# Performance work log

Measured on AMD Instinct MI355X. Metric: run time of the kernel, lower is better.

Reference implementation:

```python
import jax, jax.numpy as jnp
import numpy as np


def setup_inputs() -> dict:
    key = jax.random.key(0)
    k1, k2, k3, k4 = jax.random.split(key, 4)
    n_entity, n_rel, dim = 2048, 32, 512
    entities = jax.random.normal(k1, (n_entity, dim), dtype=jnp.float32)
    relations = jax.random.normal(k2, (n_rel, dim), dtype=jnp.float32)
    W = jax.random.normal(k3, (dim, dim), dtype=jnp.float32) * (1.0 / np.sqrt(dim))
    b = jax.random.normal(k4, (dim,), dtype=jnp.float32) * 0.01
    return {"entities": entities, "relations": relations, "W": W, "b": b}


def reference(entities, relations, W, b):
    # gate_nn applied to both entities and relations (shared Linear)
    E = entities @ W.T + b            # [n_entity, dim]
    R = relations @ W.T + b           # [n_rel, dim]
    # Diagonal RESCAL: scores[e, r, f] = sum_d E[e,d] * R[r,d] * E[f,d]
    # Equivalent to the per-relation loop E @ diag(R_r) @ E^T, fused into one einsum.
    scores = jnp.einsum('ed,rd,fd->erf', E, R, E)  # [n_entity, n_rel, n_entity]
    return scores
```

## Files before the change

### kernel.cpp

```cpp
#include <hip/hip_runtime.h>

typedef __attribute__((ext_vector_type(8))) __bf16 bf16x8;
typedef __attribute__((ext_vector_type(4))) float f32x4;

__device__ __forceinline__ float bf2f(unsigned int u) {
    return __uint_as_float(u << 16);
}
__device__ __forceinline__ unsigned short f2bf(float f) {
    unsigned int x = __float_as_uint(f);
    return (unsigned short)((x + 0x7fffu + ((x >> 16) & 1u)) >> 16);
}

__global__ void cast_all(const float* __restrict__ ent, const float* __restrict__ rel,
                         const float* __restrict__ W,
                         unsigned short* __restrict__ X_bf,
                         unsigned short* __restrict__ W_bf) {
    int i = blockIdx.x * blockDim.x + threadIdx.x;
    const float* src;
    unsigned short* dst;
    int g;
    if (i < 262144) {
        src = ent; dst = X_bf; g = i;
    } else if (i < 266240) {
        src = rel; dst = X_bf + 2048 * 512; g = i - 262144;
    } else {
        if (i >= 331776) return;
        src = W; dst = W_bf; g = i - 266240;
    }
    float4 v = reinterpret_cast<const float4*>(src)[g];
    ushort4 o;
    o.x = f2bf(v.x); o.y = f2bf(v.y); o.z = f2bf(v.z); o.w = f2bf(v.w);
    reinterpret_cast<ushort4*>(dst)[g] = o;
}

__device__ __forceinline__ unsigned int mul2bf(unsigned int a, unsigned int b) {
    float a0 = bf2f(a & 0xffffu), a1 = bf2f(a >> 16);
    float b0 = bf2f(b & 0xffffu), b1 = bf2f(b >> 16);
    return (unsigned int)f2bf(a0 * b0) | ((unsigned int)f2bf(a1 * b1) << 16);
}

__global__ void build_ap(const unsigned short* __restrict__ G,
                         unsigned short* __restrict__ Ap) {
    int t = blockIdx.x * blockDim.x + threadIdx.x;
    int row = t >> 6;
    int d = (t & 63) * 8;
    int e = row >> 5, r = row & 31;
    const uint4 ev = *reinterpret_cast<const uint4*>(G + e * 512 + d);
    const uint4 rv = *reinterpret_cast<const uint4*>(G + (2048 + r) * 512 + d);
    uint4 o;
    o.x = mul2bf(ev.x, rv.x);
    o.y = mul2bf(ev.y, rv.y);
    o.z = mul2bf(ev.z, rv.z);
    o.w = mul2bf(ev.w, rv.w);
    *reinterpret_cast<uint4*>(Ap + (size_t)row * 512 + d) = o;
}

#define BM 128
#define BN 128
#define BK 64

template <bool GUARD_M, bool BIAS_BF16OUT>
__global__ __launch_bounds__(256, 2) void mfma_gemm_bt(
    const unsigned short* __restrict__ A,
    const unsigned short* __restrict__ Bt,
    const float* __restrict__ bias,
    void* __restrict__ Cout,
    int M, int N, int K) {
    __shared__ __align__(16) unsigned short As[BM * BK];
    __shared__ __align__(16) unsigned short Bs[BN * BK];

    const int tid = threadIdx.x;
    const int lane = tid & 63;
    const int wave = tid >> 6;
    const int nbn = N / BN;
    const int bm0 = (blockIdx.x / nbn) * BM;
    const int bn0 = (blockIdx.x % nbn) * BN;
    const int wr = wave >> 1, wc = wave & 1;

    f32x4 acc[4][4] = {};

    const int srow = wave * 32 + (lane >> 3);
    const int scol = (lane & 7) * 8;

    for (int kb = 0; kb < K; kb += BK) {
#pragma unroll
        for (int i = 0; i < 4; ++i) {
            int row = bm0 + srow + i * 8;
            if (GUARD_M) row = min(row, M - 1);
            const unsigned short* src = A + (size_t)row * K + kb + scol;
            unsigned short* dst = &As[(wave * 32 + i * 8) * BK];
            __builtin_amdgcn_global_load_lds(
                (const __attribute__((address_space(1))) void*)src,
                (__attribute__((address_space(3))) void*)dst, 16, 0, 0);
        }
#pragma unroll
        for (int i = 0; i < 4; ++i) {
            int row = bn0 + srow + i * 8;
            const unsigned short* src = Bt + (size_t)row * K + kb + scol;
            unsigned short* dst = &Bs[(wave * 32 + i * 8) * BK];
            __builtin_amdgcn_global_load_lds(
                (const __attribute__((address_space(1))) void*)src,
                (__attribute__((address_space(3))) void*)dst, 16, 0, 0);
        }
        __syncthreads();

#pragma unroll
        for (int ks = 0; ks < BK / 32; ++ks) {
            const int k0 = ks * 32 + (lane >> 4) * 8;
            bf16x8 av[4], bv[4];
#pragma unroll
            for (int m = 0; m < 4; ++m)
                av[m] = *reinterpret_cast<const bf16x8*>(
                    &As[(wr * 64 + m * 16 + (lane & 15)) * BK + k0]);
#pragma unroll
            for (int n = 0; n < 4; ++n)
                bv[n] = *reinterpret_cast<const bf16x8*>(
                    &Bs[(wc * 64 + n * 16 + (lane & 15)) * BK + k0]);
#pragma unroll
            for (int m = 0; m < 4; ++m)
#pragma unroll
                for (int n = 0; n < 4; ++n)
                    acc[m][n] = __builtin_amdgcn_mfma_f32_16x16x32_bf16(
                        av[m], bv[n], acc[m][n], 0, 0, 0);
        }
        __syncthreads();
    }

#pragma unroll
    for (int m = 0; m < 4; ++m) {
#pragma unroll
        for (int n = 0; n < 4; ++n) {
#pragma unroll
            for (int j = 0; j < 4; ++j) {
                int row = bm0 + wr * 64 + m * 16 + (lane >> 4) * 4 + j;
                int col = bn0 + wc * 64 + n * 16 + (lane & 15);
                if (GUARD_M && row >= M) continue;
                float v = acc[m][n][j];
                if (BIAS_BF16OUT) {
                    v += bias[col];
                    ((unsigned short*)Cout)[(size_t)row * N + col] = f2bf(v);
                } else {
                    ((float*)Cout)[(size_t)row * N + col] = v;
                }
            }
        }
    }
}

#define NT16 16

__global__ __launch_bounds__(512, 4) void gemm128x256(
    const unsigned short* __restrict__ A,
    const unsigned short* __restrict__ B,
    float* __restrict__ C) {
    __shared__ __align__(16) unsigned short lds16[36864];

    const int tid = threadIdx.x;
    const int lane = tid & 63;
    const int wave = tid >> 6;
    const int wr = wave >> 2;
    const int wc = wave & 3;
    const int laneM = lane & 15;
    const int q = lane >> 4;
    const int laneK = q * 8;

    const int swz = (blockIdx.x & 7) * 512 + (blockIdx.x >> 3);
    const int bm0 = (swz >> 3) * 128;
    const int bn0 = (swz & 7) * 256;

    const int sr = tid >> 2;
    const int scs = ((tid & 3) * 8) ^ ((sr & 3) * 8);

    auto STAGE = [&](const unsigned short* mat, int row0, int kb, int slotU) {
        const unsigned short* src = mat + (size_t)(row0 + sr) * 512 + kb + scs;
        __builtin_amdgcn_global_load_lds(
            (const __attribute__((address_space(1))) void*)src,
            (__attribute__((address_space(3))) void*)&lds16[slotU + wave * 512],
            16, 0, 0);
    };
    auto RD = [&](int base, int rr) -> bf16x8 {
        return *reinterpret_cast<const bf16x8*>(
            &lds16[base + rr * 32 + (laneK ^ ((rr & 3) * 8))]);
    };

    f32x4 acc[4][4] = {};
    bf16x8 av[4], bv0[2], bv1[2];

    STAGE(A, bm0,        0, 0);
    STAGE(B, bn0,        0, 4096);
    STAGE(B, bn0 + 128,  0, 8192);
    STAGE(A, bm0,       32, 12288);
    STAGE(B, bn0,       32, 12288 + 4096);
    STAGE(B, bn0 + 128, 32, 12288 + 8192);
    asm volatile("s_waitcnt vmcnt(3)" ::: "memory");
    __builtin_amdgcn_s_barrier();

#pragma unroll
    for (int t = 0; t < NT16; ++t) {
        const int base = (t % 3) * 12288;
        const int nb = ((t + 2) % 3) * 12288;

#pragma unroll
        for (int m = 0; m < 4; ++m)
            av[m] = RD(base, wr * 64 + m * 16 + laneM);
#pragma unroll
        for (int n = 0; n < 2; ++n)
            bv0[n] = RD(base + 4096, wc * 64 + n * 16 + laneM);
        if (t + 2 < NT16) {
            STAGE(A, bm0, (t + 2) * 32, nb);
            STAGE(B, bn0, (t + 2) * 32, nb + 4096);
        }
        __builtin_amdgcn_s_barrier();
        asm volatile("s_waitcnt lgkmcnt(0)" ::: "memory");
        __builtin_amdgcn_sched_barrier(0);
        __builtin_amdgcn_s_setprio(1);
#pragma unroll
        for (int m = 0; m < 4; ++m)
#pragma unroll
            for (int n = 0; n < 2; ++n)
                acc[m][n] = __builtin_amdgcn_mfma_f32_16x16x32_bf16(
                    av[m], bv0[n], acc[m][n], 0, 0, 0);
        __builtin_amdgcn_s_setprio(0);
        __builtin_amdgcn_s_barrier();

#pragma unroll
        for (int n = 0; n < 2; ++n)
            bv1[n] = RD(base + 4096, wc * 64 + (2 + n) * 16 + laneM);
        if (t + 2 < NT16)
            STAGE(B, bn0 + 128, (t + 2) * 32, nb + 8192);
        __builtin_amdgcn_s_barrier();
        asm volatile("s_waitcnt lgkmcnt(0)" ::: "memory");
        __builtin_amdgcn_sched_barrier(0);
        __builtin_amdgcn_s_setprio(1);
#pragma unroll
        for (int m = 0; m < 4; ++m)
#pragma unroll
            for (int n = 0; n < 2; ++n)
                acc[m][2 + n] = __builtin_amdgcn_mfma_f32_16x16x32_bf16(
                    av[m], bv1[n], acc[m][2 + n], 0, 0, 0);
        __builtin_amdgcn_s_setprio(0);

        if (t < NT16 - 1) {
            if (t == NT16 - 2)
                asm volatile("s_waitcnt vmcnt(0)" ::: "memory");
            else
                asm volatile("s_waitcnt vmcnt(3)" ::: "memory");
            __builtin_amdgcn_s_barrier();
        }
    }

    {
        float* fb = (float*)lds16;
#pragma unroll
        for (int p = 0; p < 2; ++p) {
            __syncthreads();
            if (wr == p) {
#pragma unroll
                for (int m = 0; m < 4; ++m)
#pragma unroll
                    for (int n = 0; n < 4; ++n)
#pragma unroll
                        for (int j = 0; j < 4; ++j) {
                            int L = m * 16 + q * 4 + j;
                            int fl = wc * 64 + n * 16 + laneM;
                            fb[L * 256 + (fl ^ ((L & 12) << 2))] = acc[m][n][j];
                        }
            }
            __syncthreads();
#pragma unroll
            for (int rr = 0; rr < 2; ++rr) {
                int R = wave * 8 + rr * 4 + q;
                float* dstRow = C + (size_t)(bm0 + p * 64 + R) * 2048 + bn0;
                int sx = (R & 12) << 2;
#pragma unroll
                for (int g = 0; g < 4; ++g) {
                    int fl = g * 64 + laneM * 4;
                    f32x4 v = *reinterpret_cast<const f32x4*>(
                        &fb[R * 256 + (fl ^ sx)]);
                    __builtin_nontemporal_store(v, (f32x4*)(dstRow + fl));
                }
            }
        }
    }
}

extern "C" void kernel_launch(void* const* d_in, const int* in_sizes, int n_in,
                              void* d_out, int out_size, void* d_ws, size_t ws_size,
                              hipStream_t stream) {
    const float* entities  = (const float*)d_in[0];
    const float* relations = (const float*)d_in[1];
    const float* W         = (const float*)d_in[2];
    const float* b         = (const float*)d_in[3];

    char* ws = (char*)d_ws;
    unsigned short* W_bf = (unsigned short*)ws;
    unsigned short* X_bf = (unsigned short*)(ws + 524288);
    unsigned short* G_bf = (unsigned short*)(ws + 524288 + 2129920);
    unsigned short* Ap   = (unsigned short*)(ws + 524288 + 2129920 + 2129920);

    cast_all<<<1296, 256, 0, stream>>>(entities, relations, W, X_bf, W_bf);

    mfma_gemm_bt<true, true><<<17 * 4, 256, 0, stream>>>(
        X_bf, W_bf, b, (void*)G_bf, 2080, 512, 512);

    build_ap<<<16384, 256, 0, stream>>>(G_bf, Ap);

    gemm128x256<<<4096, 512, 0, stream>>>(Ap, G_bf, (float*)d_out);
}
```

Baseline: 203.6 us.

## Fuse E*R Hadamard product into main GEMM, drop build_ap kernel

Removes the separate build_ap kernel that materialized the 65536x512 bf16 A' = E⊙R matrix. The main GEMM now loads E and R fragments straight from G into registers, multiplies them on the fly with packed bf16 conversion, and stages only the B operand through LDS. This also cuts the per-iteration barriers from two halves to one, and shrinks LDS. It cuts the extra kernel launch and roughly 64MB of write plus read traffic, at the cost of VALU work and register pressure inside the MFMA loop. The waitcnt counts are retuned to match.

```diff
diff --git a/kernel.cpp b/kernel.cpp
--- a/kernel.cpp
+++ b/kernel.cpp
@@ -9,6 +9,27 @@
 __device__ __forceinline__ unsigned short f2bf(float f) {
     unsigned int x = __float_as_uint(f);
     return (unsigned short)((x + 0x7fffu + ((x >> 16) & 1u)) >> 16);
+}
+
+__device__ __forceinline__ unsigned int mulpack(unsigned int e, unsigned int r) {
+    float e0 = __uint_as_float(e << 16);
+    float e1 = __uint_as_float(e & 0xffff0000u);
+    float r0 = __uint_as_float(r << 16);
+    float r1 = __uint_as_float(r & 0xffff0000u);
+    float p0 = e0 * r0;
+    float p1 = e1 * r1;
+    unsigned int out;
+    asm("v_cvt_pk_bf16_f32 %0, %1, %2" : "=v"(out) : "v"(p0), "v"(p1));
+    return out;
+}
+
+__device__ __forceinline__ bf16x8 mp4(uint4 e, uint4 r) {
+    union { uint4 a; bf16x8 b; } u;
+    u.a.x = mulpack(e.x, r.x);
+    u.a.y = mulpack(e.y, r.y);
+    u.a.z = mulpack(e.z, r.z);
+    u.a.w = mulpack(e.w, r.w);
+    return u.b;
 }
 
 __global__ void cast_all(const float* __restrict__ ent, const float* __restrict__ rel,
@@ -33,28 +54,6 @@
     reinterpret_cast<ushort4*>(dst)[g] = o;
 }
 
-__device__ __forceinline__ unsigned int mul2bf(unsigned int a, unsigned int b) {
-    float a0 = bf2f(a & 0xffffu), a1 = bf2f(a >> 16);
-    float b0 = bf2f(b & 0xffffu), b1 = bf2f(b >> 16);
-    return (unsigned int)f2bf(a0 * b0) | ((unsigned int)f2bf(a1 * b1) << 16);
-}
-
-__global__ void build_ap(const unsigned short* __restrict__ G,
-                         unsigned short* __restrict__ Ap) {
-    int t = blockIdx.x * blockDim.x + threadIdx.x;
-    int row = t >> 6;
-    int d = (t & 63) * 8;
-    int e = row >> 5, r = row & 31;
-    const uint4 ev = *reinterpret_cast<const uint4*>(G + e * 512 + d);
-    const uint4 rv = *reinterpret_cast<const uint4*>(G + (2048 + r) * 512 + d);
-    uint4 o;
-    o.x = mul2bf(ev.x, rv.x);
-    o.y = mul2bf(ev.y, rv.y);
-    o.z = mul2bf(ev.z, rv.z);
-    o.w = mul2bf(ev.w, rv.w);
-    *reinterpret_cast<uint4*>(Ap + (size_t)row * 512 + d) = o;
-}
-
 #define BM 128
 #define BN 128
 #define BK 64
@@ -149,11 +148,10 @@
 
 #define NT16 16
 
-__global__ __launch_bounds__(512, 4) void gemm128x256(
-    const unsigned short* __restrict__ A,
-    const unsigned short* __restrict__ B,
+__global__ __launch_bounds__(512) void gemm_fusedA(
+    const unsigned short* __restrict__ G,
     float* __restrict__ C) {
-    __shared__ __align__(16) unsigned short lds16[36864];
+    __shared__ __align__(16) unsigned short lds16[32768];
 
     const int tid = threadIdx.x;
     const int lane = tid & 63;
@@ -171,80 +169,77 @@
     const int sr = tid >> 2;
     const int scs = ((tid & 3) * 8) ^ ((sr & 3) * 8);
 
-    auto STAGE = [&](const unsigned short* mat, int row0, int kb, int slotU) {
-        const unsigned short* src = mat + (size_t)(row0 + sr) * 512 + kb + scs;
-        __builtin_amdgcn_global_load_lds(
-            (const __attribute__((address_space(1))) void*)src,
-            (__attribute__((address_space(3))) void*)&lds16[slotU + wave * 512],
-            16, 0, 0);
+    auto STAGE_B = [&](int kb, int P) {
+#pragma unroll
+        for (int rd = 0; rd < 2; ++rd) {
+            const unsigned short* src =
+                G + (size_t)(bn0 + rd * 128 + sr) * 512 + kb + scs;
+            __builtin_amdgcn_global_load_lds(
+                (const __attribute__((address_space(1))) void*)src,
+                (__attribute__((address_space(3))) void*)
+                    &lds16[P * 8192 + rd * 4096 + wave * 512],
+                16, 0, 0);
+        }
     };
-    auto RD = [&](int base, int rr) -> bf16x8 {
+    auto RD = [&](int P, int rr) -> bf16x8 {
         return *reinterpret_cast<const bf16x8*>(
-            &lds16[base + rr * 32 + (laneK ^ ((rr & 3) * 8))]);
+            &lds16[P * 8192 + rr * 32 + (laneK ^ ((rr & 3) * 8))]);
     };
 
+    const unsigned short* Eb = G + (size_t)((bm0 >> 5) + wr * 2) * 512 + laneK;
+    const unsigned short* Rb = G + (size_t)(2048 + laneM) * 512 + laneK;
+
+    uint4 Ev[2][2], Rv[2][2];
+    auto ISSUE_ER = [&](int t) {
+        const int p = t & 1;
+#pragma unroll
+        for (int h = 0; h < 2; ++h) {
+            Ev[p][h] = *reinterpret_cast<const uint4*>(Eb + h * 512 + t * 32);
+            Rv[p][h] = *reinterpret_cast<const uint4*>(Rb + h * 16 * 512 + t * 32);
+        }
+    };
+
     f32x4 acc[4][4] = {};
-    bf16x8 av[4], bv0[2], bv1[2];
-
-    STAGE(A, bm0,        0, 0);
-    STAGE(B, bn0,        0, 4096);
-    STAGE(B, bn0 + 128,  0, 8192);
-    STAGE(A, bm0,       32, 12288);
-    STAGE(B, bn0,       32, 12288 + 4096);
-    STAGE(B, bn0 + 128, 32, 12288 + 8192);
-    asm volatile("s_waitcnt vmcnt(3)" ::: "memory");
+    bf16x8 bv[4];
+
+    ISSUE_ER(0);
+    STAGE_B(0, 0);
+    STAGE_B(32, 1);
+    asm volatile("s_waitcnt vmcnt(2)" ::: "memory");
     __builtin_amdgcn_s_barrier();
 
 #pragma unroll
     for (int t = 0; t < NT16; ++t) {
-        const int base = (t % 3) * 12288;
-        const int nb = ((t + 2) % 3) * 12288;
-
-#pragma unroll
-        for (int m = 0; m < 4; ++m)
-            av[m] = RD(base, wr * 64 + m * 16 + laneM);
-#pragma unroll
-        for (int n = 0; n < 2; ++n)
-            bv0[n] = RD(base + 4096, wc * 64 + n * 16 + laneM);
-        if (t + 2 < NT16) {
-            STAGE(A, bm0, (t + 2) * 32, nb);
-            STAGE(B, bn0, (t + 2) * 32, nb + 4096);
-        }
-        __builtin_amdgcn_s_barrier();
+        const int P = t % 3;
+
+#pragma unroll
+        for (int n = 0; n < 4; ++n)
+            bv[n] = RD(P, wc * 64 + n * 16 + laneM);
+
+        if (t + 2 < NT16)
+            STAGE_B((t + 2) * 32, (t + 2) % 3);
+        if (t + 1 < NT16)
+            ISSUE_ER(t + 1);
+
         asm volatile("s_waitcnt lgkmcnt(0)" ::: "memory");
         __builtin_amdgcn_sched_barrier(0);
+
         __builtin_amdgcn_s_setprio(1);
 #pragma unroll
-        for (int m = 0; m < 4; ++m)
-#pragma unroll
-            for (int n = 0; n < 2; ++n)
+        for (int m = 0; m < 4; ++m) {
+            bf16x8 av = mp4(Ev[t & 1][m >> 1], Rv[t & 1][m & 1]);
+#pragma unroll
+            for (int n = 0; n < 4; ++n)
                 acc[m][n] = __builtin_amdgcn_mfma_f32_16x16x32_bf16(
-                    av[m], bv0[n], acc[m][n], 0, 0, 0);
+                    av, bv[n], acc[m][n], 0, 0, 0);
+        }
         __builtin_amdgcn_s_setprio(0);
-        __builtin_amdgcn_s_barrier();
-
-#pragma unroll
-        for (int n = 0; n < 2; ++n)
-            bv1[n] = RD(base + 4096, wc * 64 + (2 + n) * 16 + laneM);
-        if (t + 2 < NT16)
-            STAGE(B, bn0 + 128, (t + 2) * 32, nb + 8192);
-        __builtin_amdgcn_s_barrier();
-        asm volatile("s_waitcnt lgkmcnt(0)" ::: "memory");
-        __builtin_amdgcn_sched_barrier(0);
-        __builtin_amdgcn_s_setprio(1);
-#pragma unroll
-        for (int m = 0; m < 4; ++m)
-#pragma unroll
-            for (int n = 0; n < 2; ++n)
-                acc[m][2 + n] = __builtin_amdgcn_mfma_f32_16x16x32_bf16(
-                    av[m], bv1[n], acc[m][2 + n], 0, 0, 0);
-        __builtin_amdgcn_s_setprio(0);
 
         if (t < NT16 - 1) {
-            if (t == NT16 - 2)
-                asm volatile("s_waitcnt vmcnt(0)" ::: "memory");
+            if (t < NT16 - 2)
+                asm volatile("s_waitcnt vmcnt(6)" ::: "memory");
             else
-                asm volatile("s_waitcnt vmcnt(3)" ::: "memory");
+                asm volatile("s_waitcnt vmcnt(4)" ::: "memory");
             __builtin_amdgcn_s_barrier();
         }
     }
@@ -296,14 +291,11 @@
     unsigned short* W_bf = (unsigned short*)ws;
     unsigned short* X_bf = (unsigned short*)(ws + 524288);
     unsigned short* G_bf = (unsigned short*)(ws + 524288 + 2129920);
-    unsigned short* Ap   = (unsigned short*)(ws + 524288 + 2129920 + 2129920);
 
     cast_all<<<1296, 256, 0, stream>>>(entities, relations, W, X_bf, W_bf);
 
     mfma_gemm_bt<true, true><<<17 * 4, 256, 0, stream>>>(
         X_bf, W_bf, b, (void*)G_bf, 2080, 512, 512);
 
-    build_ap<<<16384, 256, 0, stream>>>(G_bf, Ap);
-
-    gemm128x256<<<4096, 512, 0, stream>>>(Ap, G_bf, (float*)d_out);
-}
+    gemm_fusedA<<<4096, 512, 0, stream>>>(G_bf, (float*)d_out);
+}
```

Result: slower. 300.5 us (+47.6%).
